# Kernel tuning notes

Hardware: AMD Instinct MI355X
Metric: run time of the kernel (lower is better)

The kernel has to match this reference:

```python
import jax, jax.numpy as jnp
import numpy as np

# Approximate EMD matching (Fan et al. approxmatch): 10 annealed soft-assignment
# rounds with levels -4^j for j = 7..-1 and level 0 for the final round.
_LEVELS = jnp.asarray([-(4.0 ** j) for j in range(7, -2, -1)] + [0.0], dtype=jnp.float32)


def _approx_match(d2, n, m):
    # d2: [b, n, m] squared pairwise distances
    b = d2.shape[0]
    factorl = max(n, m) / float(n)
    factorr = max(n, m) / float(m)
    remainl0 = jnp.full((b, n), factorl, dtype=d2.dtype)
    remainr0 = jnp.full((b, m), factorr, dtype=d2.dtype)
    match0 = jnp.zeros_like(d2)

    def step(carry, level):
        match, remainl, remainr = carry
        w = jnp.exp(level * d2) * remainr[:, None, :]            # [b,n,m]
        w = w / (jnp.sum(w, axis=-1, keepdims=True) + 1e-9)      # row-normalize
        w = w * remainl[:, :, None]                              # scale by left capacity
        ss2 = jnp.sum(w, axis=1)                                 # [b,m] column mass
        s = jnp.minimum(remainr / (ss2 + 1e-9), 1.0)             # column saturation
        w = w * s[:, None, :]
        match = match + w
        remainl = jnp.maximum(remainl - jnp.sum(w, axis=-1), 0.0)
        remainr = jnp.maximum(remainr - jnp.sum(w, axis=1), 0.0)
        return (match, remainl, remainr), None

    (match, _, _), _ = jax.lax.scan(step, (match0, remainl0, remainr0), _LEVELS)
    return match


def setup_inputs() -> dict:
    key = jax.random.key(0)
    k1, k2 = jax.random.split(key)
    xyz1 = jax.random.normal(k1, (16, 2048, 3), dtype=jnp.float32)
    xyz2 = jax.random.normal(k2, (16, 2048, 3), dtype=jnp.float32)
    return {"xyz1": xyz1, "xyz2": xyz2}


def reference(xyz1, xyz2):
    n, m = xyz1.shape[1], xyz2.shape[1]
    diff = xyz1[:, :, None, :] - xyz2[:, None, :, :]             # [b,n,m,3]
    d2 = jnp.sum(diff * diff, axis=-1)                           # [b,n,m]
    match = _approx_match(d2, n, m)
    dist = jnp.sqrt(jnp.maximum(d2, 1e-12))
    cost = jnp.sum(match * dist, axis=(1, 2))                    # [b]
    return cost
```

## Files before the change

kernel.cpp:

```cpp
#include <hip/hip_runtime.h>
#include <math.h>

#define B 16
#define N 2048
#define M 2048
#define BN (B * N)
#define LOG2E 1.4426950408889634f

#define CJ 128
#define NCH (M / CJ)
#define TPB 128
#define RPT 4
#define RBLK (TPB * RPT)

typedef float v2f __attribute__((ext_vector_type(2)));

#define EXP2F(x) __builtin_amdgcn_exp2f(x)
#define SQRTF(x) __builtin_amdgcn_sqrtf(x)

__device__ inline v2f exp2v(v2f a) {
    v2f r;
    r.x = EXP2F(a.x);
    r.y = EXP2F(a.y);
    return r;
}

__global__ __launch_bounds__(256) void k_pack(const float* __restrict__ xyz1,
                                              const float* __restrict__ xyz2,
                                              float4* __restrict__ p1,
                                              float4* __restrict__ p2,
                                              float4* __restrict__ p2s,
                                              float c20) {
    int idx = blockIdx.x * 256 + threadIdx.x;
    const float* s = (idx < BN) ? (xyz1 + 3 * (size_t)idx)
                                : (xyz2 + 3 * (size_t)(idx - BN));
    float x = s[0], y = s[1], z = s[2];
    float n = fmaf(x, x, fmaf(y, y, z * z));
    float4 v = make_float4(x, y, z, n);
    if (idx < BN) {
        p1[idx] = v;
    } else {
        p2[idx - BN] = v;
        p2s[idx - BN] = make_float4(x, y, z, c20 * n);
    }
}

__global__ __launch_bounds__(256) void k_init(float* __restrict__ rl0,
                                              float* __restrict__ rr0,
                                              float* __restrict__ rs0,
                                              float* __restrict__ rs2,
                                              float* __restrict__ t1b,
                                              float* __restrict__ ss20,
                                              float* __restrict__ cost) {
    int idx = blockIdx.x * 256 + threadIdx.x;
    rl0[idx] = 1.0f;
    rr0[idx] = 1.0f;
    rs0[idx] = 0.0f;
    rs2[idx] = 0.0f;
    t1b[idx] = 0.0f;
    ss20[idx] = 0.0f;
    if (idx < B) cost[idx] = 0.0f;
}

__global__ __launch_bounds__(TPB, 2) void k_rowsum0(const float4* __restrict__ p1,
                                                    const float4* __restrict__ p2s,
                                                    float* __restrict__ rs,
                                                    float c2) {
    const int b = blockIdx.z;
    const int tx = threadIdx.x;
    const int i0 = blockIdx.y * RBLK + tx;
    const float4* __restrict__ g = p2s + b * M + blockIdx.x * CJ;

    float4 fa = p1[b * N + i0];
    float4 fb = p1[b * N + i0 + TPB];
    float4 fc = p1[b * N + i0 + 2 * TPB];
    float4 fd = p1[b * N + i0 + 3 * TPB];
    const float m2c = -2.0f * c2;
    v2f Xp0 = {m2c * fa.x, m2c * fb.x}, Xp1 = {m2c * fc.x, m2c * fd.x};
    v2f Yp0 = {m2c * fa.y, m2c * fb.y}, Yp1 = {m2c * fc.y, m2c * fd.y};
    v2f Zp0 = {m2c * fa.z, m2c * fb.z}, Zp1 = {m2c * fc.z, m2c * fd.z};
    v2f ni0 = {c2 * fa.w, c2 * fb.w}, ni1 = {c2 * fc.w, c2 * fd.w};

    v2f acc0 = {0.0f, 0.0f}, acc1 = {0.0f, 0.0f};
#pragma unroll 8
    for (int t = 0; t < CJ; ++t) {
        float4 q4 = g[t];
        v2f arg0 = q4.x * Xp0 + (q4.y * Yp0 + (q4.z * Zp0 + (ni0 + q4.w)));
        v2f arg1 = q4.x * Xp1 + (q4.y * Yp1 + (q4.z * Zp1 + (ni1 + q4.w)));
        acc0 += exp2v(arg0);
        acc1 += exp2v(arg1);
    }
    atomicAdd(&rs[b * N + i0], acc0.x);
    atomicAdd(&rs[b * N + i0 + TPB], acc0.y);
    atomicAdd(&rs[b * N + i0 + 2 * TPB], acc1.x);
    atomicAdd(&rs[b * N + i0 + 3 * TPB], acc1.y);
}

__global__ __launch_bounds__(TPB, 2) void k_colsum(const float4* __restrict__ p1,
                                                   const float4* __restrict__ p2,
                                                   const float* __restrict__ rl_in,
                                                   float* __restrict__ rl_out,
                                                   const float* __restrict__ rs_prev,
                                                   const float* __restrict__ rs_cur,
                                                   float* __restrict__ rs_zero,
                                                   const float* __restrict__ t1_in,
                                                   float* __restrict__ t1_zero,
                                                   const float* __restrict__ rr,
                                                   float* __restrict__ ss2_acc,
                                                   float cS) {
    __shared__ float2 tileC[CJ];
    const int b = blockIdx.z;
    const int tx = threadIdx.x;
    const int j0 = blockIdx.y * RBLK + tx;

    {
        int gi = b * N + blockIdx.x * CJ + tx;
        float4 f = p1[gi];
        float rlo = rl_in[gi];
        float ap = rlo / (rs_prev[gi] + 1e-9f);
        float rln = fmaxf(rlo - ap * t1_in[gi], 0.0f);
        float a = rln / (rs_cur[gi] + 1e-9f);
        tileC[tx] = make_float2(a, cS * f.w);
        if (blockIdx.y == 0) {
            rl_out[gi] = rln;
            t1_zero[gi] = 0.0f;
            rs_zero[gi] = 0.0f;
        }
    }
    __syncthreads();

    const float4* __restrict__ g = p1 + b * N + blockIdx.x * CJ;

    float4 fa = p2[b * M + j0];
    float4 fb = p2[b * M + j0 + TPB];
    float4 fc = p2[b * M + j0 + 2 * TPB];
    float4 fd = p2[b * M + j0 + 3 * TPB];
    const float m2c = -2.0f * cS;
    v2f Xp0 = {m2c * fa.x, m2c * fb.x}, Xp1 = {m2c * fc.x, m2c * fd.x};
    v2f Yp0 = {m2c * fa.y, m2c * fb.y}, Yp1 = {m2c * fc.y, m2c * fd.y};
    v2f Zp0 = {m2c * fa.z, m2c * fb.z}, Zp1 = {m2c * fc.z, m2c * fd.z};
    v2f nj0 = {cS * fa.w, cS * fb.w}, nj1 = {cS * fc.w, cS * fd.w};

    v2f acc0 = {0.0f, 0.0f}, acc1 = {0.0f, 0.0f};
#pragma unroll 8
    for (int t = 0; t < CJ; ++t) {
        float4 q4 = g[t];
        float2 cv = tileC[t];
        v2f arg0 = q4.x * Xp0 + (q4.y * Yp0 + (q4.z * Zp0 + (nj0 + cv.y)));
        v2f arg1 = q4.x * Xp1 + (q4.y * Yp1 + (q4.z * Zp1 + (nj1 + cv.y)));
        acc0 += exp2v(arg0) * cv.x;
        acc1 += exp2v(arg1) * cv.x;
    }
    atomicAdd(&ss2_acc[b * M + j0], acc0.x * rr[b * M + j0]);
    atomicAdd(&ss2_acc[b * M + j0 + TPB], acc0.y * rr[b * M + j0 + TPB]);
    atomicAdd(&ss2_acc[b * M + j0 + 2 * TPB], acc1.x * rr[b * M + j0 + 2 * TPB]);
    atomicAdd(&ss2_acc[b * M + j0 + 3 * TPB], acc1.y * rr[b * M + j0 + 3 * TPB]);
}

__global__ __launch_bounds__(256) void k_suma(const float* __restrict__ rl_in,
                                              float* __restrict__ rl_out,
                                              const float* __restrict__ rs_prev,
                                              const float* __restrict__ rs_cur,
                                              const float* __restrict__ t1_in,
                                              float* __restrict__ S) {
    __shared__ float red[4];
    const int b = blockIdx.x;
    const int tx = threadIdx.x;
    float s = 0.0f;
#pragma unroll
    for (int k = 0; k < N / 256; ++k) {
        int gi = b * N + k * 256 + tx;
        float rlo = rl_in[gi];
        float ap = rlo / (rs_prev[gi] + 1e-9f);
        float rln = fmaxf(rlo - ap * t1_in[gi], 0.0f);
        rl_out[gi] = rln;
        s += rln / (rs_cur[gi] + 1e-9f);
    }
#pragma unroll
    for (int off = 32; off > 0; off >>= 1)
        s += __shfl_down(s, off, 64);
    if ((tx & 63) == 0) red[tx >> 6] = s;
    __syncthreads();
    if (tx == 0) S[b] = red[0] + red[1] + red[2] + red[3];
}

__global__ __launch_bounds__(256) void k_mulss2(const float* __restrict__ rr,
                                                const float* __restrict__ S,
                                                float* __restrict__ ss2_out) {
    int idx = blockIdx.x * 256 + threadIdx.x;
    ss2_out[idx] = rr[idx] * S[idx >> 11];
}

__global__ __launch_bounds__(256) void k_prepf(const float4* __restrict__ p2,
                                               const float* __restrict__ rr_in,
                                               float* __restrict__ rr_out,
                                               const float* __restrict__ ss2_in,
                                               float* __restrict__ ss2_zero,
                                               float4* __restrict__ F4,
                                               float cS) {
    int j = blockIdx.x * 256 + threadIdx.x;
    float4 f = p2[j];
    float rrv = rr_in[j];
    float sv = ss2_in[j];
    float s = fminf(rrv / (sv + 1e-9f), 1.0f);
    float q = rrv * s;
    float rrn = fmaxf(rrv - sv * s, 0.0f);
    F4[j] = make_float4(q, rrn, cS * f.w, 0.0f);
    rr_out[j] = rrn;
    ss2_zero[j] = 0.0f;
}

template <int MODE>
__global__ __launch_bounds__(TPB, 2) void k_fused(const float4* __restrict__ p1,
                                                  const float4* __restrict__ p2,
                                                  const float4* __restrict__ F4,
                                                  const float* __restrict__ rl_new,
                                                  const float* __restrict__ rs_cur,
                                                  float* __restrict__ rs_next,
                                                  float* __restrict__ t1_acc,
                                                  float* __restrict__ cost,
                                                  float cS, float invS) {
    const int b = blockIdx.z;
    const int tx = threadIdx.x;
    const int i0 = blockIdx.y * RBLK + tx;
    const float4* __restrict__ g = p2 + b * M + blockIdx.x * CJ;
    const float4* __restrict__ h = F4 + b * M + blockIdx.x * CJ;

    float4 fa = p1[b * N + i0];
    float4 fb = p1[b * N + i0 + TPB];
    float4 fc = p1[b * N + i0 + 2 * TPB];
    float4 fd = p1[b * N + i0 + 3 * TPB];
    const float m2c = -2.0f * cS;
    v2f Xp0 = {m2c * fa.x, m2c * fb.x}, Xp1 = {m2c * fc.x, m2c * fd.x};
    v2f Yp0 = {m2c * fa.y, m2c * fb.y}, Yp1 = {m2c * fc.y, m2c * fd.y};
    v2f Zp0 = {m2c * fa.z, m2c * fb.z}, Zp1 = {m2c * fc.z, m2c * fd.z};
    v2f ni0 = {cS * fa.w, cS * fb.w}, ni1 = {cS * fc.w, cS * fd.w};

    v2f T10 = {0.0f, 0.0f}, T20 = {0.0f, 0.0f}, rs0v = {0.0f, 0.0f};
    v2f T11 = {0.0f, 0.0f}, T21 = {0.0f, 0.0f}, rs1v = {0.0f, 0.0f};
#pragma unroll 8
    for (int t = 0; t < CJ; ++t) {
        float4 q4 = g[t];
        float4 f4 = h[t];
        v2f arg0 = q4.x * Xp0 + (q4.y * Yp0 + (q4.z * Zp0 + (ni0 + f4.z)));
        v2f arg1 = q4.x * Xp1 + (q4.y * Yp1 + (q4.z * Zp1 + (ni1 + f4.z)));
        v2f el0, el1, en0, en1;
        if (MODE == 0) {
            en0 = exp2v(arg0);
            en1 = exp2v(arg1);
            v2f e20 = en0 * en0, e21 = en1 * en1;
            el0 = e20 * e20;
            el1 = e21 * e21;
        } else if (MODE == 1) {
            el0 = exp2v(arg0);
            el1 = exp2v(arg1);
        }
        v2f d20 = arg0 * invS, d21 = arg1 * invS;
        d20.x = fmaxf(d20.x, 1e-12f);
        d20.y = fmaxf(d20.y, 1e-12f);
        d21.x = fmaxf(d21.x, 1e-12f);
        d21.y = fmaxf(d21.y, 1e-12f);
        v2f sd0, sd1;
        sd0.x = SQRTF(d20.x);
        sd0.y = SQRTF(d20.y);
        sd1.x = SQRTF(d21.x);
        sd1.y = SQRTF(d21.y);
        v2f wq0, wq1;
        if (MODE == 2) {
            wq0.x = f4.x; wq0.y = f4.x;
            wq1.x = f4.x; wq1.y = f4.x;
        } else {
            wq0 = el0 * f4.x;
            wq1 = el1 * f4.x;
        }
        T10 += wq0;
        T11 += wq1;
        T20 += wq0 * sd0;
        T21 += wq1 * sd1;
        if (MODE == 0) {
            rs0v += en0 * f4.y;
            rs1v += en1 * f4.y;
        } else if (MODE == 1) {
            rs0v += f4.y;
            rs1v += f4.y;
        }
    }

    const int gi0 = b * N + i0;
    if (MODE != 2) {
        atomicAdd(&t1_acc[gi0], T10.x);
        atomicAdd(&t1_acc[gi0 + TPB], T10.y);
        atomicAdd(&t1_acc[gi0 + 2 * TPB], T11.x);
        atomicAdd(&t1_acc[gi0 + 3 * TPB], T11.y);
        atomicAdd(&rs_next[gi0], rs0v.x);
        atomicAdd(&rs_next[gi0 + TPB], rs0v.y);
        atomicAdd(&rs_next[gi0 + 2 * TPB], rs1v.x);
        atomicAdd(&rs_next[gi0 + 3 * TPB], rs1v.y);
    }

    float aa = rl_new[gi0] / (rs_cur[gi0] + 1e-9f);
    float ab = rl_new[gi0 + TPB] / (rs_cur[gi0 + TPB] + 1e-9f);
    float ac = rl_new[gi0 + 2 * TPB] / (rs_cur[gi0 + 2 * TPB] + 1e-9f);
    float ad = rl_new[gi0 + 3 * TPB] / (rs_cur[gi0 + 3 * TPB] + 1e-9f);
    float contrib = fmaf(aa, T20.x, fmaf(ab, T20.y, fmaf(ac, T21.x, ad * T21.y)));
#pragma unroll
    for (int off = 32; off > 0; off >>= 1)
        contrib += __shfl_down(contrib, off, 64);
    if ((threadIdx.x & 63) == 0) atomicAdd(&cost[b], contrib);
}

extern "C" void kernel_launch(void* const* d_in, const int* in_sizes, int n_in,
                              void* d_out, int out_size, void* d_ws, size_t ws_size,
                              hipStream_t stream) {
    const float* xyz1 = (const float*)d_in[0];
    const float* xyz2 = (const float*)d_in[1];
    float* cost = (float*)d_out;

    float* ws = (float*)d_ws;
    float* rl[2] = {ws + 0 * BN, ws + 1 * BN};
    float* rr[2] = {ws + 2 * BN, ws + 3 * BN};
    float* rs[3] = {ws + 4 * BN, ws + 5 * BN, ws + 6 * BN};
    float* ss2b[2] = {ws + 7 * BN, ws + 8 * BN};
    float* t1[2] = {ws + 9 * BN, ws + 10 * BN};
    float4* p1 = (float4*)(ws + 11 * BN);
    float4* p2 = (float4*)(ws + 15 * BN);
    float4* p2s = (float4*)(ws + 19 * BN);
    float4* F4 = (float4*)(ws + 23 * BN);
    float* S = ws + 27 * BN;

    static const float levels[10] = {-16384.0f, -4096.0f, -1024.0f, -256.0f,
                                     -64.0f,    -16.0f,   -4.0f,    -1.0f,
                                     -0.25f,    0.0f};
    float c2[10];
    for (int l = 0; l < 10; ++l) c2[l] = levels[l] * LOG2E;

    dim3 grid(NCH, N / RBLK, B);
    dim3 blk(TPB);

    k_pack<<<dim3(2 * BN / 256), dim3(256), 0, stream>>>(xyz1, xyz2, p1, p2,
                                                         p2s, c2[0]);
    k_init<<<dim3(BN / 256), dim3(256), 0, stream>>>(rl[0], rr[0], rs[0], rs[2],
                                                     t1[1], ss2b[0], cost);
    k_rowsum0<<<grid, blk, 0, stream>>>(p1, p2s, rs[0], c2[0]);

    for (int l = 0; l < 10; ++l) {
        int p = l & 1;
        if (l < 9) {
            k_colsum<<<grid, blk, 0, stream>>>(
                p1, p2, rl[p], rl[1 - p], rs[(l + 2) % 3], rs[l % 3],
                rs[(l + 1) % 3], t1[1 - p], t1[p], rr[p], ss2b[p], c2[l]);
        } else {
            k_suma<<<dim3(B), dim3(256), 0, stream>>>(
                rl[p], rl[1 - p], rs[(l + 2) % 3], rs[l % 3], t1[1 - p], S);
            k_mulss2<<<dim3(BN / 256), dim3(256), 0, stream>>>(rr[p], S, ss2b[p]);
        }

        float cS = (l <= 7) ? c2[l + 1] : ((l == 8) ? c2[8] : 1.0f);
        float invS = (l <= 8) ? (1.0f / cS) : 1.0f;

        k_prepf<<<dim3(BN / 256), dim3(256), 0, stream>>>(
            p2, rr[p], rr[1 - p], ss2b[p], ss2b[1 - p], F4, cS);

        if (l <= 7) {
            k_fused<0><<<grid, blk, 0, stream>>>(p1, p2, F4, rl[1 - p],
                                                 rs[l % 3], rs[(l + 1) % 3],
                                                 t1[p], cost, cS, invS);
        } else if (l == 8) {
            k_fused<1><<<grid, blk, 0, stream>>>(p1, p2, F4, rl[1 - p],
                                                 rs[l % 3], rs[(l + 1) % 3],
                                                 t1[p], cost, cS, invS);
        } else {
            k_fused<2><<<grid, blk, 0, stream>>>(p1, p2, F4, rl[1 - p],
                                                 rs[l % 3], rs[(l + 1) % 3],
                                                 t1[p], cost, cS, invS);
        }
    }
}
```

Before: 626.3 us.

## Morton-sort points and skip tiles whose bounding-box distance underflows exp

Replaces the pack kernel with a per-batch bitonic sort of points by Morton code, so spatially close points sit in the same tiles. It then computes per-tile bounding boxes and has the rowsum, colsum and fused kernels return early when the minimum squared distance between the row block and column tile is large enough that exp(level*d2) falls below about 2^-151, which is zero in fp32. This aims to avoid exp and accumulation work in the sharp early annealing rounds. The cost is an extra sort and bbox pass, and divergent early exits; the skip is exact only within fp32 underflow, and the atomics, which are unordered, sum in a different order.

```diff
diff --git a/kernel.cpp b/kernel.cpp
--- a/kernel.cpp
+++ b/kernel.cpp
@@ -25,23 +25,111 @@
     return r;
 }
 
-__global__ __launch_bounds__(256) void k_pack(const float* __restrict__ xyz1,
-                                              const float* __restrict__ xyz2,
-                                              float4* __restrict__ p1,
-                                              float4* __restrict__ p2,
-                                              float4* __restrict__ p2s,
-                                              float c20) {
-    int idx = blockIdx.x * 256 + threadIdx.x;
-    const float* s = (idx < BN) ? (xyz1 + 3 * (size_t)idx)
-                                : (xyz2 + 3 * (size_t)(idx - BN));
-    float x = s[0], y = s[1], z = s[2];
-    float n = fmaf(x, x, fmaf(y, y, z * z));
-    float4 v = make_float4(x, y, z, n);
-    if (idx < BN) {
-        p1[idx] = v;
-    } else {
-        p2[idx - BN] = v;
-        p2s[idx - BN] = make_float4(x, y, z, c20 * n);
+__device__ inline float bbox_d2min(float4 amn, float4 amx, float4 bmn, float4 bmx) {
+    float gx = fmaxf(0.0f, fmaxf(amn.x - bmx.x, bmn.x - amx.x));
+    float gy = fmaxf(0.0f, fmaxf(amn.y - bmx.y, bmn.y - amx.y));
+    float gz = fmaxf(0.0f, fmaxf(amn.z - bmx.z, bmn.z - amx.z));
+    return fmaf(gx, gx, fmaf(gy, gy, gz * gz));
+}
+
+__global__ __launch_bounds__(1024) void k_sort(const float* __restrict__ xyz1,
+                                               const float* __restrict__ xyz2,
+                                               float4* __restrict__ p1,
+                                               float4* __restrict__ p2,
+                                               float4* __restrict__ p2s,
+                                               float c20) {
+    __shared__ unsigned long long keys[2048];
+    const int b = blockIdx.x;
+    const int side = blockIdx.y;
+    const int t = threadIdx.x;
+    const float* src = (side ? xyz2 : xyz1) + (size_t)b * N * 3;
+
+    for (int p = t; p < 2048; p += 1024) {
+        float x = src[3 * p], y = src[3 * p + 1], z = src[3 * p + 2];
+        unsigned ux = (unsigned)fminf(fmaxf((x + 6.0f) * 85.3333f, 0.0f), 1023.0f);
+        unsigned uy = (unsigned)fminf(fmaxf((y + 6.0f) * 85.3333f, 0.0f), 1023.0f);
+        unsigned uz = (unsigned)fminf(fmaxf((z + 6.0f) * 85.3333f, 0.0f), 1023.0f);
+        unsigned m = 0;
+#define SPREAD(v)                                                      \
+    ({                                                                 \
+        unsigned s = (v);                                              \
+        s = (s | (s << 16)) & 0x030000FFu;                             \
+        s = (s | (s << 8)) & 0x0300F00Fu;                              \
+        s = (s | (s << 4)) & 0x030C30C3u;                              \
+        s = (s | (s << 2)) & 0x09249249u;                              \
+        s;                                                             \
+    })
+        m = SPREAD(ux) | (SPREAD(uy) << 1) | (SPREAD(uz) << 2);
+#undef SPREAD
+        keys[p] = ((unsigned long long)m << 11) | (unsigned)p;
+    }
+    __syncthreads();
+
+    for (unsigned k = 2; k <= 2048; k <<= 1) {
+        for (unsigned j = k >> 1; j > 0; j >>= 1) {
+            for (int p = t; p < 2048; p += 1024) {
+                unsigned q = (unsigned)p ^ j;
+                if (q > (unsigned)p) {
+                    unsigned long long a = keys[p], c = keys[q];
+                    bool up = ((p & k) == 0);
+                    if (up ? (a > c) : (a < c)) {
+                        keys[p] = c;
+                        keys[q] = a;
+                    }
+                }
+            }
+            __syncthreads();
+        }
+    }
+
+    for (int p = t; p < 2048; p += 1024) {
+        int idx = (int)(keys[p] & 2047u);
+        float x = src[3 * idx], y = src[3 * idx + 1], z = src[3 * idx + 2];
+        float n = fmaf(x, x, fmaf(y, y, z * z));
+        float4 v = make_float4(x, y, z, n);
+        if (side) {
+            p2[b * M + p] = v;
+            p2s[b * M + p] = make_float4(x, y, z, c20 * n);
+        } else {
+            p1[b * N + p] = v;
+        }
+    }
+}
+
+__global__ __launch_bounds__(64) void k_bbox(const float4* __restrict__ p1,
+                                             const float4* __restrict__ p2,
+                                             float4* __restrict__ BB128,
+                                             float4* __restrict__ BB512) {
+    __shared__ float4 mn[16], mx[16];
+    const int b = blockIdx.x;
+    const int side = blockIdx.y;
+    const int t = threadIdx.x;
+    const float4* src = (side ? p2 : p1) + b * 2048;
+
+    if (t < 16) {
+        float4 lo = make_float4(1e30f, 1e30f, 1e30f, 0.0f);
+        float4 hi = make_float4(-1e30f, -1e30f, -1e30f, 0.0f);
+        for (int i = 0; i < 128; ++i) {
+            float4 v = src[t * 128 + i];
+            lo.x = fminf(lo.x, v.x); lo.y = fminf(lo.y, v.y); lo.z = fminf(lo.z, v.z);
+            hi.x = fmaxf(hi.x, v.x); hi.y = fmaxf(hi.y, v.y); hi.z = fmaxf(hi.z, v.z);
+        }
+        mn[t] = lo; mx[t] = hi;
+        int o = ((side * B + b) * 16 + t) * 2;
+        BB128[o] = lo;
+        BB128[o + 1] = hi;
+    }
+    __syncthreads();
+    if (t < 4) {
+        float4 lo = mn[4 * t], hi = mx[4 * t];
+        for (int i = 1; i < 4; ++i) {
+            float4 a = mn[4 * t + i], c = mx[4 * t + i];
+            lo.x = fminf(lo.x, a.x); lo.y = fminf(lo.y, a.y); lo.z = fminf(lo.z, a.z);
+            hi.x = fmaxf(hi.x, c.x); hi.y = fmaxf(hi.y, c.y); hi.z = fmaxf(hi.z, c.z);
+        }
+        int o = ((side * B + b) * 4 + t) * 2;
+        BB512[o] = lo;
+        BB512[o + 1] = hi;
     }
 }
 
@@ -65,8 +153,16 @@
 __global__ __launch_bounds__(TPB, 2) void k_rowsum0(const float4* __restrict__ p1,
                                                     const float4* __restrict__ p2s,
                                                     float* __restrict__ rs,
-                                                    float c2) {
+                                                    const float4* __restrict__ bbRows,
+                                                    const float4* __restrict__ bbTile,
+                                                    float d2skip, float c2) {
     const int b = blockIdx.z;
+    {
+        int ro = (b * 4 + blockIdx.y) * 2;
+        int to = (b * 16 + blockIdx.x) * 2;
+        float d2min = bbox_d2min(bbRows[ro], bbRows[ro + 1], bbTile[to], bbTile[to + 1]);
+        if (d2min >= d2skip) return;
+    }
     const int tx = threadIdx.x;
     const int i0 = blockIdx.y * RBLK + tx;
     const float4* __restrict__ g = p2s + b * M + blockIdx.x * CJ;
@@ -107,26 +203,37 @@
                                                    float* __restrict__ t1_zero,
                                                    const float* __restrict__ rr,
                                                    float* __restrict__ ss2_acc,
-                                                   float cS) {
+                                                   const float4* __restrict__ bbRows,
+                                                   const float4* __restrict__ bbTile,
+                                                   float d2skip, float cS) {
     __shared__ float2 tileC[CJ];
     const int b = blockIdx.z;
     const int tx = threadIdx.x;
     const int j0 = blockIdx.y * RBLK + tx;
 
+    bool skip;
     {
+        int ro = (b * 4 + blockIdx.y) * 2;
+        int to = (b * 16 + blockIdx.x) * 2;
+        float d2min = bbox_d2min(bbRows[ro], bbRows[ro + 1], bbTile[to], bbTile[to + 1]);
+        skip = (d2min >= d2skip);
+    }
+
+    if (!skip || blockIdx.y == 0) {
         int gi = b * N + blockIdx.x * CJ + tx;
         float4 f = p1[gi];
         float rlo = rl_in[gi];
         float ap = rlo / (rs_prev[gi] + 1e-9f);
         float rln = fmaxf(rlo - ap * t1_in[gi], 0.0f);
         float a = rln / (rs_cur[gi] + 1e-9f);
-        tileC[tx] = make_float2(a, cS * f.w);
         if (blockIdx.y == 0) {
             rl_out[gi] = rln;
             t1_zero[gi] = 0.0f;
             rs_zero[gi] = 0.0f;
         }
-    }
+        if (!skip) tileC[tx] = make_float2(a, cS * f.w);
+    }
+    if (skip) return;
     __syncthreads();
 
     const float4* __restrict__ g = p1 + b * N + blockIdx.x * CJ;
@@ -219,8 +326,16 @@
                                                   float* __restrict__ rs_next,
                                                   float* __restrict__ t1_acc,
                                                   float* __restrict__ cost,
-                                                  float cS, float invS) {
+                                                  const float4* __restrict__ bbRows,
+                                                  const float4* __restrict__ bbTile,
+                                                  float d2skip, float cS, float invS) {
     const int b = blockIdx.z;
+    if (MODE == 0) {
+        int ro = (b * 4 + blockIdx.y) * 2;
+        int to = (b * 16 + blockIdx.x) * 2;
+        float d2min = bbox_d2min(bbRows[ro], bbRows[ro + 1], bbTile[to], bbTile[to + 1]);
+        if (d2min >= d2skip) return;
+    }
     const int tx = threadIdx.x;
     const int i0 = blockIdx.y * RBLK + tx;
     const float4* __restrict__ g = p2 + b * M + blockIdx.x * CJ;
@@ -327,6 +442,12 @@
     float4* p2s = (float4*)(ws + 19 * BN);
     float4* F4 = (float4*)(ws + 23 * BN);
     float* S = ws + 27 * BN;
+    float4* BB128 = (float4*)(ws + 27 * BN + 64);
+    float4* BB512 = BB128 + 1024;
+    const float4* bbRowsF = BB512;
+    const float4* bbTileF = BB128 + 512;
+    const float4* bbRowsC = BB512 + 128;
+    const float4* bbTileC = BB128;
 
     static const float levels[10] = {-16384.0f, -4096.0f, -1024.0f, -256.0f,
                                      -64.0f,    -16.0f,   -4.0f,    -1.0f,
@@ -337,18 +458,21 @@
     dim3 grid(NCH, N / RBLK, B);
     dim3 blk(TPB);
 
-    k_pack<<<dim3(2 * BN / 256), dim3(256), 0, stream>>>(xyz1, xyz2, p1, p2,
-                                                         p2s, c2[0]);
+    k_sort<<<dim3(B, 2), dim3(1024), 0, stream>>>(xyz1, xyz2, p1, p2, p2s, c2[0]);
+    k_bbox<<<dim3(B, 2), dim3(64), 0, stream>>>(p1, p2, BB128, BB512);
     k_init<<<dim3(BN / 256), dim3(256), 0, stream>>>(rl[0], rr[0], rs[0], rs[2],
                                                      t1[1], ss2b[0], cost);
-    k_rowsum0<<<grid, blk, 0, stream>>>(p1, p2s, rs[0], c2[0]);
+    k_rowsum0<<<grid, blk, 0, stream>>>(p1, p2s, rs[0], bbRowsF, bbTileF,
+                                        151.0f / fabsf(c2[0]), c2[0]);
 
     for (int l = 0; l < 10; ++l) {
         int p = l & 1;
         if (l < 9) {
+            float dsC = 151.0f / fabsf(c2[l]);
             k_colsum<<<grid, blk, 0, stream>>>(
                 p1, p2, rl[p], rl[1 - p], rs[(l + 2) % 3], rs[l % 3],
-                rs[(l + 1) % 3], t1[1 - p], t1[p], rr[p], ss2b[p], c2[l]);
+                rs[(l + 1) % 3], t1[1 - p], t1[p], rr[p], ss2b[p],
+                bbRowsC, bbTileC, dsC, c2[l]);
         } else {
             k_suma<<<dim3(B), dim3(256), 0, stream>>>(
                 rl[p], rl[1 - p], rs[(l + 2) % 3], rs[l % 3], t1[1 - p], S);
@@ -357,6 +481,7 @@
 
         float cS = (l <= 7) ? c2[l + 1] : ((l == 8) ? c2[8] : 1.0f);
         float invS = (l <= 8) ? (1.0f / cS) : 1.0f;
+        float dsF = (l <= 7) ? 151.0f / fabsf(c2[l + 1]) : 1e30f;
 
         k_prepf<<<dim3(BN / 256), dim3(256), 0, stream>>>(
             p2, rr[p], rr[1 - p], ss2b[p], ss2b[1 - p], F4, cS);
@@ -364,15 +489,18 @@
         if (l <= 7) {
             k_fused<0><<<grid, blk, 0, stream>>>(p1, p2, F4, rl[1 - p],
                                                  rs[l % 3], rs[(l + 1) % 3],
-                                                 t1[p], cost, cS, invS);
+                                                 t1[p], cost, bbRowsF, bbTileF,
+                                                 dsF, cS, invS);
         } else if (l == 8) {
             k_fused<1><<<grid, blk, 0, stream>>>(p1, p2, F4, rl[1 - p],
                                                  rs[l % 3], rs[(l + 1) % 3],
-                                                 t1[p], cost, cS, invS);
+                                                 t1[p], cost, bbRowsF, bbTileF,
+                                                 dsF, cS, invS);
         } else {
             k_fused<2><<<grid, blk, 0, stream>>>(p1, p2, F4, rl[1 - p],
                                                  rs[l % 3], rs[(l + 1) % 3],
-                                                 t1[p], cost, cS, invS);
-        }
-    }
-}
+                                                 t1[p], cost, bbRowsF, bbTileF,
+                                                 dsF, cS, invS);
+        }
+    }
+}
```

After: 683.2 us. 1.09x slower.
